# Kernel optimization log

Hardware: AMD Instinct MI355X
Metric: run time of the kernel (lower is better)

Reference implementation:

```python
import jax, jax.numpy as jnp
import numpy as np

B, T_OBS, T_FUT, D, H = 8192, 128, 64, 5, 128


def _gru_step(h, x, Wih, Whh, bih, bhh):
    # PyTorch GRU math, gate order (r, z, n) in the stacked [3H, *] weights.
    gi = x @ Wih.T + bih          # [B, 3H]
    gh = h @ Whh.T + bhh          # [B, 3H]
    ir, iz, inn = jnp.split(gi, 3, axis=-1)
    hr, hz, hn = jnp.split(gh, 3, axis=-1)
    r = jax.nn.sigmoid(ir + hr)
    z = jax.nn.sigmoid(iz + hz)
    n = jnp.tanh(inn + r * hn)
    return (1.0 - z) * n + z * h


def setup_inputs() -> dict:
    key = jax.random.key(0)
    ks = jax.random.split(key, 12)
    s = 0.1  # modest init scale to keep gates in a sane range
    return {
        "obs": jax.random.normal(ks[0], (B, T_OBS, D), jnp.float32),
        "target": jax.random.normal(ks[1], (B, T_FUT, D), jnp.float32),
        "enc_Wih": jax.random.normal(ks[2], (3 * H, D), jnp.float32) * s,
        "enc_Whh": jax.random.normal(ks[3], (3 * H, H), jnp.float32) * s,
        "enc_bih": jax.random.normal(ks[4], (3 * H,), jnp.float32) * s,
        "enc_bhh": jax.random.normal(ks[5], (3 * H,), jnp.float32) * s,
        "cell_Wih": jax.random.normal(ks[6], (3 * H, D), jnp.float32) * s,
        "cell_Whh": jax.random.normal(ks[7], (3 * H, H), jnp.float32) * s,
        "cell_bih": jax.random.normal(ks[8], (3 * H,), jnp.float32) * s,
        "cell_bhh": jax.random.normal(ks[9], (3 * H,), jnp.float32) * s,
        "head_W": jax.random.normal(ks[10], (D, H), jnp.float32) * s,
        "head_b": jax.random.normal(ks[11], (D,), jnp.float32) * s,
    }


def reference(obs, target, enc_Wih, enc_Whh, enc_bih, enc_bhh,
              cell_Wih, cell_Whh, cell_bih, cell_bhh, head_W, head_b):
    b = obs.shape[0]
    h0 = jnp.zeros((b, H), obs.dtype)

    # --- encoder: GRU over obs, keep only final hidden state ---
    def enc_step(h, x):
        h_new = _gru_step(h, x, enc_Wih, enc_Whh, enc_bih, enc_bhh)
        return h_new, None
    hT, _ = jax.lax.scan(enc_step, h0, jnp.swapaxes(obs, 0, 1))  # xs: [T_obs, B, D]

    # --- teacher-forced rollout: x_0 = obs[:, -1], x_t = target[:, t-1] ---
    xs = jnp.concatenate([obs[:, -1:, :], target[:, :-1, :]], axis=1)  # [B, T_fut, D]
    def roll_step(h, x):
        h_new = _gru_step(h, x, cell_Wih, cell_Whh, cell_bih, cell_bhh)
        return h_new, h_new
    _, hs = jax.lax.scan(roll_step, hT, jnp.swapaxes(xs, 0, 1))  # hs: [T_fut, B, H]

    preds = jnp.einsum('tbh,dh->tbd', hs, head_W) + head_b  # [T_fut, B, D]
    return jnp.swapaxes(preds, 0, 1)  # [B, T_fut, D]
```

## Files before the change

kernel.cpp:

```cpp
#include <hip/hip_runtime.h>

#define B_TOT 8192
#define T_OBS 128
#define T_FUT 64
#define T_ALL 192
#define DIN 5
#define HD 128
#define BT 32
#define LDSTR 136

#define LOG2E 1.44269504088896340736f

typedef __attribute__((ext_vector_type(8))) short short8;
typedef __attribute__((ext_vector_type(4))) float f32x4;
typedef __attribute__((ext_vector_type(2))) unsigned int u32x2;
typedef __attribute__((ext_vector_type(4))) unsigned int u32x4;

__device__ inline short f2bf(float f) {
    unsigned u = __float_as_uint(f);
    u += 0x7FFFu + ((u >> 16) & 1u);
    return (short)(u >> 16);
}

__device__ inline unsigned cvtpk(float lo, float hi) {
    unsigned r;
    asm volatile("v_cvt_pk_bf16_f32 %0, %1, %2" : "=v"(r) : "v"(lo), "v"(hi));
    return r;
}

__device__ inline f32x4 MFMA(short8 a, short8 b, f32x4 c) {
    return __builtin_amdgcn_mfma_f32_16x16x32_bf16(a, b, c, 0, 0, 0);
}

__device__ inline short8 load_w8s(const float* p, float s) {
    float4 a = *reinterpret_cast<const float4*>(p);
    float4 b = *reinterpret_cast<const float4*>(p + 4);
    short8 r;
    r[0] = f2bf(a.x * s); r[1] = f2bf(a.y * s); r[2] = f2bf(a.z * s); r[3] = f2bf(a.w * s);
    r[4] = f2bf(b.x * s); r[5] = f2bf(b.y * s); r[6] = f2bf(b.z * s); r[7] = f2bf(b.w * s);
    return r;
}
__device__ inline short8 load_w5s(const float* p, float s) {
    short8 r = (short8)0;
    r[0] = f2bf(p[0] * s); r[1] = f2bf(p[1] * s); r[2] = f2bf(p[2] * s);
    r[3] = f2bf(p[3] * s); r[4] = f2bf(p[4] * s);
    return r;
}

__global__ __launch_bounds__(512, 1)
void gru_tracemodel_kernel(const float* __restrict__ obs, const float* __restrict__ target,
                           const float* __restrict__ eWih, const float* __restrict__ eWhh,
                           const float* __restrict__ ebih, const float* __restrict__ ebhh,
                           const float* __restrict__ cWih, const float* __restrict__ cWhh,
                           const float* __restrict__ cbih, const float* __restrict__ cbhh,
                           const float* __restrict__ headW, const float* __restrict__ headb,
                           float* __restrict__ out)
{
    __shared__ __attribute__((aligned(16))) short Abuf[2][BT][LDSTR];

    const int tid   = threadIdx.x;
    const int wave  = tid >> 6;
    const int lane  = tid & 63;
    const int q     = lane >> 4;
    const int c     = lane & 15;
    const int b0    = blockIdx.x * BT;
    const int wbase = wave * 16;

    for (int i = tid; i < 2 * BT * LDSTR; i += 512) ((short*)Abuf)[i] = 0;

    short8 Wr[5], Wz[5], Wn[5];
    f32x4  br4, bz4, bnh4, bni4;

    auto load_phase = [&](const float* Wih, const float* Whh,
                          const float* bih, const float* bhh) {
        const int nr = 0 * HD + wbase + c;
        const int nz = 1 * HD + wbase + c;
        const int nn = 2 * HD + wbase + c;
        #pragma unroll
        for (int kt = 0; kt < 4; ++kt) {
            Wr[kt] = load_w8s(Whh + nr * HD + kt * 32 + q * 8, LOG2E);
            Wz[kt] = load_w8s(Whh + nz * HD + kt * 32 + q * 8, LOG2E);
            Wn[kt] = load_w8s(Whh + nn * HD + kt * 32 + q * 8, 2.f * LOG2E);
        }
        Wr[4] = (q == 0) ? load_w5s(Wih + nr * DIN, LOG2E) : (short8)0;
        Wz[4] = (q == 0) ? load_w5s(Wih + nz * DIN, LOG2E) : (short8)0;
        Wn[4] = (q == 0) ? load_w5s(Wih + nn * DIN, 2.f * LOG2E) : (short8)0;
        const int n0 = wbase + q * 4;
        #pragma unroll
        for (int r = 0; r < 4; ++r) {
            br4[r]  = (bih[0 * HD + n0 + r] + bhh[0 * HD + n0 + r]) * LOG2E;
            bz4[r]  = (bih[1 * HD + n0 + r] + bhh[1 * HD + n0 + r]) * LOG2E;
            bni4[r] = bih[2 * HD + n0 + r] * (2.f * LOG2E);
            bnh4[r] = bhh[2 * HD + n0 + r] * (2.f * LOG2E);
        }
    };
    load_phase(eWih, eWhh, ebih, ebhh);

    short8 Whd[4];
    f32x4  hb4;
    #pragma unroll
    for (int kt = 0; kt < 4; ++kt)
        Whd[kt] = (c < DIN) ? load_w8s(headW + c * HD + kt * 32 + q * 8, 1.f) : (short8)0;
    #pragma unroll
    for (int r = 0; r < 4; ++r)
        hb4[r] = (q * 4 + r < DIN) ? headb[q * 4 + r] : 0.f;

    float hreg[2][4] = {{0.f,0.f,0.f,0.f},{0.f,0.f,0.f,0.f}};

    const float* obsr[2] = { obs + (size_t)(b0 + c) * (T_OBS * DIN),
                             obs + (size_t)(b0 + 16 + c) * (T_OBS * DIN) };
    const float* tgtr[2] = { target + (size_t)(b0 + c) * (T_FUT * DIN),
                             target + (size_t)(b0 + 16 + c) * (T_FUT * DIN) };
    float x5[2][5] = {{0,0,0,0,0},{0,0,0,0,0}};
    if (q == 0) {
        #pragma unroll
        for (int a = 0; a < 2; ++a)
            #pragma unroll
            for (int j = 0; j < DIN; ++j) x5[a][j] = obsr[a][j];
    }

    for (int t = 0; t <= T_ALL; ++t) {
        __syncthreads();
        const int p = t & 1;

        short8 ah[2][4];
        #pragma unroll
        for (int a = 0; a < 2; ++a) {
            const short* ap = &Abuf[p][a * 16 + c][0];
            #pragma unroll
            for (int kt = 0; kt < 4; ++kt)
                ah[a][kt] = *reinterpret_cast<const short8*>(ap + kt * 32 + q * 8);
        }

        if (t >= T_OBS + 1 && wave == ((t - T_OBS - 1) & 7)) {
            const int s = t - (T_OBS + 1);
            const int d0 = q * 4;
            #pragma unroll
            for (int a = 0; a < 2; ++a) {
                f32x4 acc = hb4;
                #pragma unroll
                for (int kt = 0; kt < 4; ++kt)
                    acc = MFMA(Whd[kt], ah[a][kt], acc);
                if (d0 < DIN) {
                    float* op = out + ((size_t)(b0 + a * 16 + c) * T_FUT + s) * DIN + d0;
                    op[0] = acc[0];
                    if (q == 0) { op[1] = acc[1]; op[2] = acc[2]; op[3] = acc[3]; }
                }
            }
        }
        if (t == T_ALL) break;

        if (t == T_OBS) load_phase(cWih, cWhh, cbih, cbhh);

        short8 ax[2];
        {
            unsigned u0a = 0, u1a = 0, u2a = 0, u0b = 0, u1b = 0, u2b = 0;
            if (q == 0) {
                u0a = cvtpk(x5[0][0], x5[0][1]);
                u1a = cvtpk(x5[0][2], x5[0][3]);
                u2a = cvtpk(x5[0][4], 0.f);
                u0b = cvtpk(x5[1][0], x5[1][1]);
                u1b = cvtpk(x5[1][2], x5[1][3]);
                u2b = cvtpk(x5[1][4], 0.f);
            }
            u32x4 va = {u0a, u1a, u2a, 0u};
            u32x4 vb = {u0b, u1b, u2b, 0u};
            ax[0] = __builtin_bit_cast(short8, va);
            ax[1] = __builtin_bit_cast(short8, vb);
            const int tn = t + 1;
            if (q == 0 && tn < T_ALL) {
                #pragma unroll
                for (int a = 0; a < 2; ++a) {
                    const float* px = (tn < T_OBS)  ? (obsr[a] + tn * DIN)
                                    : (tn == T_OBS) ? (obsr[a] + (T_OBS - 1) * DIN)
                                                    : (tgtr[a] + (tn - T_OBS - 1) * DIN);
                    #pragma unroll
                    for (int j = 0; j < DIN; ++j) x5[a][j] = px[j];
                }
            }
        }

        #pragma unroll
        for (int a = 0; a < 2; ++a) {
            f32x4 aR  = br4;
            f32x4 aZ  = bz4;
            f32x4 aNh = bnh4;
            f32x4 aNi = bni4;
            #pragma unroll
            for (int kt = 0; kt < 4; ++kt) {
                aR  = MFMA(Wr[kt], ah[a][kt], aR);
                aZ  = MFMA(Wz[kt], ah[a][kt], aZ);
                aNh = MFMA(Wn[kt], ah[a][kt], aNh);
            }
            aR  = MFMA(Wr[4], ax[a], aR);
            aZ  = MFMA(Wz[4], ax[a], aZ);
            aNi = MFMA(Wn[4], ax[a], aNi);

            float hn[4];
            #pragma unroll
            for (int r = 0; r < 4; ++r) {
                float rv = __builtin_amdgcn_rcpf(1.f + __builtin_amdgcn_exp2f(-aR[r]));
                float zv = __builtin_amdgcn_rcpf(1.f + __builtin_amdgcn_exp2f(-aZ[r]));
                float yv = fmaf(rv, aNh[r], aNi[r]);
                float nv = 1.f - 2.f * __builtin_amdgcn_rcpf(1.f + __builtin_amdgcn_exp2f(yv));
                float h_ = nv + zv * (hreg[a][r] - nv);
                hreg[a][r] = h_;
                hn[r] = h_;
            }
            u32x2 wv = { cvtpk(hn[0], hn[1]), cvtpk(hn[2], hn[3]) };
            *reinterpret_cast<u32x2*>(&Abuf[1 - p][a * 16 + c][wbase + q * 4]) = wv;
        }
    }
}

extern "C" void kernel_launch(void* const* d_in, const int* in_sizes, int n_in,
                              void* d_out, int out_size, void* d_ws, size_t ws_size,
                              hipStream_t stream)
{
    (void)in_sizes; (void)n_in; (void)d_ws; (void)ws_size; (void)out_size;
    gru_tracemodel_kernel<<<dim3(B_TOT / BT), dim3(512), 0, stream>>>(
        (const float*)d_in[0],  (const float*)d_in[1],
        (const float*)d_in[2],  (const float*)d_in[3],
        (const float*)d_in[4],  (const float*)d_in[5],
        (const float*)d_in[6],  (const float*)d_in[7],
        (const float*)d_in[8],  (const float*)d_in[9],
        (const float*)d_in[10], (const float*)d_in[11],
        (float*)d_out);
}
```

Baseline: 338.1 us.

## Split waves by batch half and hidden slice; fuse GRU gate nonlinearities

```diff
diff --git a/kernel.cpp b/kernel.cpp
--- a/kernel.cpp
+++ b/kernel.cpp
@@ -64,34 +64,39 @@
     const int q     = lane >> 4;
     const int c     = lane & 15;
     const int b0    = blockIdx.x * BT;
-    const int wbase = wave * 16;
+    const int s4    = wave & 3;
+    const int a     = wave >> 2;
+    const int nbase = s4 * 32;
 
     for (int i = tid; i < 2 * BT * LDSTR; i += 512) ((short*)Abuf)[i] = 0;
 
-    short8 Wr[5], Wz[5], Wn[5];
-    f32x4  br4, bz4, bnh4, bni4;
+    short8 Wr[2][5], Wz[2][5], Wn[2][5];
+    f32x4  br4[2], bz4[2], bnh4[2], bni4[2];
 
     auto load_phase = [&](const float* Wih, const float* Whh,
                           const float* bih, const float* bhh) {
-        const int nr = 0 * HD + wbase + c;
-        const int nz = 1 * HD + wbase + c;
-        const int nn = 2 * HD + wbase + c;
-        #pragma unroll
-        for (int kt = 0; kt < 4; ++kt) {
-            Wr[kt] = load_w8s(Whh + nr * HD + kt * 32 + q * 8, LOG2E);
-            Wz[kt] = load_w8s(Whh + nz * HD + kt * 32 + q * 8, LOG2E);
-            Wn[kt] = load_w8s(Whh + nn * HD + kt * 32 + q * 8, 2.f * LOG2E);
-        }
-        Wr[4] = (q == 0) ? load_w5s(Wih + nr * DIN, LOG2E) : (short8)0;
-        Wz[4] = (q == 0) ? load_w5s(Wih + nz * DIN, LOG2E) : (short8)0;
-        Wn[4] = (q == 0) ? load_w5s(Wih + nn * DIN, 2.f * LOG2E) : (short8)0;
-        const int n0 = wbase + q * 4;
-        #pragma unroll
-        for (int r = 0; r < 4; ++r) {
-            br4[r]  = (bih[0 * HD + n0 + r] + bhh[0 * HD + n0 + r]) * LOG2E;
-            bz4[r]  = (bih[1 * HD + n0 + r] + bhh[1 * HD + n0 + r]) * LOG2E;
-            bni4[r] = bih[2 * HD + n0 + r] * (2.f * LOG2E);
-            bnh4[r] = bhh[2 * HD + n0 + r] * (2.f * LOG2E);
+        #pragma unroll
+        for (int g = 0; g < 2; ++g) {
+            const int nr = 0 * HD + nbase + 16 * g + c;
+            const int nz = 1 * HD + nbase + 16 * g + c;
+            const int nn = 2 * HD + nbase + 16 * g + c;
+            #pragma unroll
+            for (int kt = 0; kt < 4; ++kt) {
+                Wr[g][kt] = load_w8s(Whh + nr * HD + kt * 32 + q * 8, LOG2E);
+                Wz[g][kt] = load_w8s(Whh + nz * HD + kt * 32 + q * 8, LOG2E);
+                Wn[g][kt] = load_w8s(Whh + nn * HD + kt * 32 + q * 8, 2.f * LOG2E);
+            }
+            Wr[g][4] = (q == 0) ? load_w5s(Wih + nr * DIN, LOG2E) : (short8)0;
+            Wz[g][4] = (q == 0) ? load_w5s(Wih + nz * DIN, LOG2E) : (short8)0;
+            Wn[g][4] = (q == 0) ? load_w5s(Wih + nn * DIN, 2.f * LOG2E) : (short8)0;
+            const int n0 = nbase + 16 * g + q * 4;
+            #pragma unroll
+            for (int r = 0; r < 4; ++r) {
+                br4[g][r]  = (bih[0 * HD + n0 + r] + bhh[0 * HD + n0 + r]) * LOG2E;
+                bz4[g][r]  = (bih[1 * HD + n0 + r] + bhh[1 * HD + n0 + r]) * LOG2E;
+                bni4[g][r] = bih[2 * HD + n0 + r] * (2.f * LOG2E);
+                bnh4[g][r] = bhh[2 * HD + n0 + r] * (2.f * LOG2E);
+            }
         }
     };
     load_phase(eWih, eWhh, ebih, ebhh);
@@ -107,108 +112,95 @@
 
     float hreg[2][4] = {{0.f,0.f,0.f,0.f},{0.f,0.f,0.f,0.f}};
 
-    const float* obsr[2] = { obs + (size_t)(b0 + c) * (T_OBS * DIN),
-                             obs + (size_t)(b0 + 16 + c) * (T_OBS * DIN) };
-    const float* tgtr[2] = { target + (size_t)(b0 + c) * (T_FUT * DIN),
-                             target + (size_t)(b0 + 16 + c) * (T_FUT * DIN) };
-    float x5[2][5] = {{0,0,0,0,0},{0,0,0,0,0}};
+    const float* obsr = obs    + (size_t)(b0 + a * 16 + c) * (T_OBS * DIN);
+    const float* tgtr = target + (size_t)(b0 + a * 16 + c) * (T_FUT * DIN);
+    float x5[5] = {0, 0, 0, 0, 0};
     if (q == 0) {
         #pragma unroll
-        for (int a = 0; a < 2; ++a)
-            #pragma unroll
-            for (int j = 0; j < DIN; ++j) x5[a][j] = obsr[a][j];
+        for (int j = 0; j < DIN; ++j) x5[j] = obsr[j];
     }
 
     for (int t = 0; t <= T_ALL; ++t) {
         __syncthreads();
         const int p = t & 1;
 
-        short8 ah[2][4];
-        #pragma unroll
-        for (int a = 0; a < 2; ++a) {
-            const short* ap = &Abuf[p][a * 16 + c][0];
-            #pragma unroll
-            for (int kt = 0; kt < 4; ++kt)
-                ah[a][kt] = *reinterpret_cast<const short8*>(ap + kt * 32 + q * 8);
-        }
-
-        if (t >= T_OBS + 1 && wave == ((t - T_OBS - 1) & 7)) {
+        short8 ah[4];
+        const short* ap = &Abuf[p][a * 16 + c][0];
+        #pragma unroll
+        for (int kt = 0; kt < 4; ++kt)
+            ah[kt] = *reinterpret_cast<const short8*>(ap + kt * 32 + q * 8);
+
+        if (t >= T_OBS + 1 && s4 == ((t - T_OBS - 1) & 3)) {
             const int s = t - (T_OBS + 1);
             const int d0 = q * 4;
-            #pragma unroll
-            for (int a = 0; a < 2; ++a) {
-                f32x4 acc = hb4;
-                #pragma unroll
-                for (int kt = 0; kt < 4; ++kt)
-                    acc = MFMA(Whd[kt], ah[a][kt], acc);
-                if (d0 < DIN) {
-                    float* op = out + ((size_t)(b0 + a * 16 + c) * T_FUT + s) * DIN + d0;
-                    op[0] = acc[0];
-                    if (q == 0) { op[1] = acc[1]; op[2] = acc[2]; op[3] = acc[3]; }
-                }
+            f32x4 acc = hb4;
+            #pragma unroll
+            for (int kt = 0; kt < 4; ++kt)
+                acc = MFMA(Whd[kt], ah[kt], acc);
+            if (d0 < DIN) {
+                float* op = out + ((size_t)(b0 + a * 16 + c) * T_FUT + s) * DIN + d0;
+                op[0] = acc[0];
+                if (q == 0) { op[1] = acc[1]; op[2] = acc[2]; op[3] = acc[3]; }
             }
         }
         if (t == T_ALL) break;
 
         if (t == T_OBS) load_phase(cWih, cWhh, cbih, cbhh);
 
-        short8 ax[2];
+        short8 ax;
         {
-            unsigned u0a = 0, u1a = 0, u2a = 0, u0b = 0, u1b = 0, u2b = 0;
+            unsigned u0 = 0, u1 = 0, u2 = 0;
             if (q == 0) {
-                u0a = cvtpk(x5[0][0], x5[0][1]);
-                u1a = cvtpk(x5[0][2], x5[0][3]);
-                u2a = cvtpk(x5[0][4], 0.f);
-                u0b = cvtpk(x5[1][0], x5[1][1]);
-                u1b = cvtpk(x5[1][2], x5[1][3]);
-                u2b = cvtpk(x5[1][4], 0.f);
-            }
-            u32x4 va = {u0a, u1a, u2a, 0u};
-            u32x4 vb = {u0b, u1b, u2b, 0u};
-            ax[0] = __builtin_bit_cast(short8, va);
-            ax[1] = __builtin_bit_cast(short8, vb);
+                u0 = cvtpk(x5[0], x5[1]);
+                u1 = cvtpk(x5[2], x5[3]);
+                u2 = cvtpk(x5[4], 0.f);
+            }
+            u32x4 va = {u0, u1, u2, 0u};
+            ax = __builtin_bit_cast(short8, va);
             const int tn = t + 1;
             if (q == 0 && tn < T_ALL) {
+                const float* px = (tn < T_OBS)  ? (obsr + tn * DIN)
+                                : (tn == T_OBS) ? (obsr + (T_OBS - 1) * DIN)
+                                                : (tgtr + (tn - T_OBS - 1) * DIN);
                 #pragma unroll
-                for (int a = 0; a < 2; ++a) {
-                    const float* px = (tn < T_OBS)  ? (obsr[a] + tn * DIN)
-                                    : (tn == T_OBS) ? (obsr[a] + (T_OBS - 1) * DIN)
-                                                    : (tgtr[a] + (tn - T_OBS - 1) * DIN);
-                    #pragma unroll
-                    for (int j = 0; j < DIN; ++j) x5[a][j] = px[j];
-                }
-            }
-        }
-
-        #pragma unroll
-        for (int a = 0; a < 2; ++a) {
-            f32x4 aR  = br4;
-            f32x4 aZ  = bz4;
-            f32x4 aNh = bnh4;
-            f32x4 aNi = bni4;
-            #pragma unroll
-            for (int kt = 0; kt < 4; ++kt) {
-                aR  = MFMA(Wr[kt], ah[a][kt], aR);
-                aZ  = MFMA(Wz[kt], ah[a][kt], aZ);
-                aNh = MFMA(Wn[kt], ah[a][kt], aNh);
-            }
-            aR  = MFMA(Wr[4], ax[a], aR);
-            aZ  = MFMA(Wz[4], ax[a], aZ);
-            aNi = MFMA(Wn[4], ax[a], aNi);
+                for (int j = 0; j < DIN; ++j) x5[j] = px[j];
+            }
+        }
+
+        #pragma unroll
+        for (int g = 0; g < 2; ++g) {
+            f32x4 aR  = MFMA(Wr[g][0], ah[0], br4[g]);
+            f32x4 aZ  = MFMA(Wz[g][0], ah[0], bz4[g]);
+            f32x4 aNh = MFMA(Wn[g][0], ah[0], bnh4[g]);
+            #pragma unroll
+            for (int kt = 1; kt < 4; ++kt) {
+                aR  = MFMA(Wr[g][kt], ah[kt], aR);
+                aZ  = MFMA(Wz[g][kt], ah[kt], aZ);
+                aNh = MFMA(Wn[g][kt], ah[kt], aNh);
+            }
+            aR  = MFMA(Wr[g][4], ax, aR);
+            aZ  = MFMA(Wz[g][4], ax, aZ);
+            f32x4 aNi = MFMA(Wn[g][4], ax, bni4[g]);
 
             float hn[4];
             #pragma unroll
             for (int r = 0; r < 4; ++r) {
-                float rv = __builtin_amdgcn_rcpf(1.f + __builtin_amdgcn_exp2f(-aR[r]));
-                float zv = __builtin_amdgcn_rcpf(1.f + __builtin_amdgcn_exp2f(-aZ[r]));
-                float yv = fmaf(rv, aNh[r], aNi[r]);
-                float nv = 1.f - 2.f * __builtin_amdgcn_rcpf(1.f + __builtin_amdgcn_exp2f(yv));
-                float h_ = nv + zv * (hreg[a][r] - nv);
-                hreg[a][r] = h_;
+                float er  = __builtin_amdgcn_exp2f(-aR[r]);
+                float rv  = __builtin_amdgcn_rcpf(1.f + er);
+                float yv  = fmaf(rv, aNh[r], aNi[r]);
+                float ey  = __builtin_amdgcn_exp2f(yv);
+                float ez  = __builtin_amdgcn_exp2f(-aZ[r]);
+                float d2  = 1.f + ey;
+                float d1  = 1.f + ez;
+                float em1 = ey - 1.f;
+                float num = fmaf(ez, em1, hreg[g][r] * d2);
+                float h_  = num * __builtin_amdgcn_rcpf(d1 * d2);
+                hreg[g][r] = h_;
                 hn[r] = h_;
             }
             u32x2 wv = { cvtpk(hn[0], hn[1]), cvtpk(hn[2], hn[3]) };
-            *reinterpret_cast<u32x2*>(&Abuf[1 - p][a * 16 + c][wbase + q * 4]) = wv;
+            *reinterpret_cast<u32x2*>(
+                &Abuf[1 - p][a * 16 + c][nbase + 16 * g + q * 4]) = wv;
         }
     }
 }
```

After: 852.9 us. 2.52x slower.

## Split GRU time loop into phases and fuse gate reciprocals into one

Applied to the files above, without the earlier changes.

```diff
diff --git a/kernel.cpp b/kernel.cpp
--- a/kernel.cpp
+++ b/kernel.cpp
@@ -114,103 +114,128 @@
     float x5[2][5] = {{0,0,0,0,0},{0,0,0,0,0}};
     if (q == 0) {
         #pragma unroll
-        for (int a = 0; a < 2; ++a)
-            #pragma unroll
-            for (int j = 0; j < DIN; ++j) x5[a][j] = obsr[a][j];
+        for (int a = 0; a < 2; ++a) {
+            float4 v4 = *reinterpret_cast<const float4*>(obsr[a]);
+            x5[a][0] = v4.x; x5[a][1] = v4.y; x5[a][2] = v4.z; x5[a][3] = v4.w;
+            x5[a][4] = obsr[a][4];
+        }
     }
 
-    for (int t = 0; t <= T_ALL; ++t) {
-        __syncthreads();
-        const int p = t & 1;
-
-        short8 ah[2][4];
+#define GRU_STEP(T, DO_HEAD, ENC)                                              \
+  {                                                                            \
+    __syncthreads();                                                           \
+    const int p_ = (T) & 1;                                                    \
+    short8 ah[2][4];                                                           \
+    _Pragma("unroll")                                                          \
+    for (int a = 0; a < 2; ++a) {                                              \
+      const short* ap = &Abuf[p_][a * 16 + c][0];                              \
+      _Pragma("unroll")                                                        \
+      for (int kt = 0; kt < 4; ++kt)                                           \
+        ah[a][kt] = *reinterpret_cast<const short8*>(ap + kt * 32 + q * 8);    \
+    }                                                                          \
+    if (DO_HEAD) {                                                             \
+      const int s_ = (T) - (T_OBS + 1);                                        \
+      if (wave == (s_ & 7)) {                                                  \
+        const int d0 = q * 4;                                                  \
+        _Pragma("unroll")                                                      \
+        for (int a = 0; a < 2; ++a) {                                          \
+          f32x4 acc = hb4;                                                     \
+          _Pragma("unroll")                                                    \
+          for (int kt = 0; kt < 4; ++kt)                                       \
+            acc = MFMA(Whd[kt], ah[a][kt], acc);                               \
+          if (d0 < DIN) {                                                      \
+            float* op = out + ((size_t)(b0 + a * 16 + c) * T_FUT + s_) * DIN + d0; \
+            op[0] = acc[0];                                                    \
+            if (q == 0) { op[1] = acc[1]; op[2] = acc[2]; op[3] = acc[3]; }    \
+          }                                                                    \
+        }                                                                      \
+      }                                                                        \
+    }                                                                          \
+    short8 ax[2];                                                              \
+    {                                                                          \
+      u32x4 va = { cvtpk(x5[0][0], x5[0][1]), cvtpk(x5[0][2], x5[0][3]),       \
+                   cvtpk(x5[0][4], 0.f), 0u };                                 \
+      u32x4 vb = { cvtpk(x5[1][0], x5[1][1]), cvtpk(x5[1][2], x5[1][3]),       \
+                   cvtpk(x5[1][4], 0.f), 0u };                                 \
+      ax[0] = __builtin_bit_cast(short8, va);                                  \
+      ax[1] = __builtin_bit_cast(short8, vb);                                  \
+      if (q == 0) {                                                            \
+        const int tn_ = (T) + 1;                                               \
+        _Pragma("unroll")                                                      \
+        for (int a = 0; a < 2; ++a) {                                          \
+          const float* px = (ENC)                                              \
+              ? (obsr[a] + ((tn_ < T_OBS) ? tn_ : (T_OBS - 1)) * DIN)          \
+              : (tgtr[a] + (tn_ - T_OBS - 1) * DIN);                           \
+          float4 v4 = *reinterpret_cast<const float4*>(px);                    \
+          x5[a][0] = v4.x; x5[a][1] = v4.y; x5[a][2] = v4.z; x5[a][3] = v4.w;  \
+          x5[a][4] = px[4];                                                    \
+        }                                                                      \
+      }                                                                        \
+    }                                                                          \
+    _Pragma("unroll")                                                          \
+    for (int a = 0; a < 2; ++a) {                                              \
+      f32x4 aR  = MFMA(Wr[0], ah[a][0], br4);                                  \
+      f32x4 aZ  = MFMA(Wz[0], ah[a][0], bz4);                                  \
+      f32x4 aNh = MFMA(Wn[0], ah[a][0], bnh4);                                 \
+      _Pragma("unroll")                                                        \
+      for (int kt = 1; kt < 4; ++kt) {                                         \
+        aR  = MFMA(Wr[kt], ah[a][kt], aR);                                     \
+        aZ  = MFMA(Wz[kt], ah[a][kt], aZ);                                     \
+        aNh = MFMA(Wn[kt], ah[a][kt], aNh);                                    \
+      }                                                                        \
+      aR  = MFMA(Wr[4], ax[a], aR);                                            \
+      aZ  = MFMA(Wz[4], ax[a], aZ);                                            \
+      f32x4 aNi = MFMA(Wn[4], ax[a], bni4);                                    \
+      float hn[4];                                                             \
+      _Pragma("unroll")                                                        \
+      for (int r = 0; r < 4; ++r) {                                            \
+        float er  = __builtin_amdgcn_exp2f(-aR[r]);                            \
+        float rv  = __builtin_amdgcn_rcpf(1.f + er);                           \
+        float yv  = fmaf(rv, aNh[r], aNi[r]);                                  \
+        float ey  = __builtin_amdgcn_exp2f(yv);                                \
+        float ez  = __builtin_amdgcn_exp2f(-aZ[r]);                            \
+        float d2  = 1.f + ey;                                                  \
+        float d1  = 1.f + ez;                                                  \
+        float em1 = ey - 1.f;                                                  \
+        float num = fmaf(ez, em1, hreg[a][r] * d2);                            \
+        float h_  = num * __builtin_amdgcn_rcpf(d1 * d2);                      \
+        hreg[a][r] = h_;                                                       \
+        hn[r] = h_;                                                            \
+      }                                                                        \
+      u32x2 wv = { cvtpk(hn[0], hn[1]), cvtpk(hn[2], hn[3]) };                 \
+      *reinterpret_cast<u32x2*>(&Abuf[1 - p_][a * 16 + c][wbase + q * 4]) = wv;\
+    }                                                                          \
+  }
+
+    for (int t = 0; t < T_OBS; ++t) GRU_STEP(t, 0, 1);
+
+    load_phase(cWih, cWhh, cbih, cbhh);
+    GRU_STEP(T_OBS, 0, 0);
+
+    for (int t = T_OBS + 1; t < T_ALL; ++t) GRU_STEP(t, 1, 0);
+
+    __syncthreads();
+    if (wave == ((T_FUT - 1) & 7)) {
+        const int p_ = T_ALL & 1;
+        const int s_ = T_FUT - 1;
+        const int d0 = q * 4;
         #pragma unroll
         for (int a = 0; a < 2; ++a) {
-            const short* ap = &Abuf[p][a * 16 + c][0];
-            #pragma unroll
-            for (int kt = 0; kt < 4; ++kt)
-                ah[a][kt] = *reinterpret_cast<const short8*>(ap + kt * 32 + q * 8);
-        }
-
-        if (t >= T_OBS + 1 && wave == ((t - T_OBS - 1) & 7)) {
-            const int s = t - (T_OBS + 1);
-            const int d0 = q * 4;
-            #pragma unroll
-            for (int a = 0; a < 2; ++a) {
-                f32x4 acc = hb4;
-                #pragma unroll
-                for (int kt = 0; kt < 4; ++kt)
-                    acc = MFMA(Whd[kt], ah[a][kt], acc);
-                if (d0 < DIN) {
-                    float* op = out + ((size_t)(b0 + a * 16 + c) * T_FUT + s) * DIN + d0;
-                    op[0] = acc[0];
-                    if (q == 0) { op[1] = acc[1]; op[2] = acc[2]; op[3] = acc[3]; }
-                }
-            }
-        }
-        if (t == T_ALL) break;
-
-        if (t == T_OBS) load_phase(cWih, cWhh, cbih, cbhh);
-
-        short8 ax[2];
-        {
-            unsigned u0a = 0, u1a = 0, u2a = 0, u0b = 0, u1b = 0, u2b = 0;
-            if (q == 0) {
-                u0a = cvtpk(x5[0][0], x5[0][1]);
-                u1a = cvtpk(x5[0][2], x5[0][3]);
-                u2a = cvtpk(x5[0][4], 0.f);
-                u0b = cvtpk(x5[1][0], x5[1][1]);
-                u1b = cvtpk(x5[1][2], x5[1][3]);
-                u2b = cvtpk(x5[1][4], 0.f);
-            }
-            u32x4 va = {u0a, u1a, u2a, 0u};
-            u32x4 vb = {u0b, u1b, u2b, 0u};
-            ax[0] = __builtin_bit_cast(short8, va);
-            ax[1] = __builtin_bit_cast(short8, vb);
-            const int tn = t + 1;
-            if (q == 0 && tn < T_ALL) {
-                #pragma unroll
-                for (int a = 0; a < 2; ++a) {
-                    const float* px = (tn < T_OBS)  ? (obsr[a] + tn * DIN)
-                                    : (tn == T_OBS) ? (obsr[a] + (T_OBS - 1) * DIN)
-                                                    : (tgtr[a] + (tn - T_OBS - 1) * DIN);
-                    #pragma unroll
-                    for (int j = 0; j < DIN; ++j) x5[a][j] = px[j];
-                }
-            }
-        }
-
-        #pragma unroll
-        for (int a = 0; a < 2; ++a) {
-            f32x4 aR  = br4;
-            f32x4 aZ  = bz4;
-            f32x4 aNh = bnh4;
-            f32x4 aNi = bni4;
+            const short* ap = &Abuf[p_][a * 16 + c][0];
+            f32x4 acc = hb4;
             #pragma unroll
             for (int kt = 0; kt < 4; ++kt) {
-                aR  = MFMA(Wr[kt], ah[a][kt], aR);
-                aZ  = MFMA(Wz[kt], ah[a][kt], aZ);
-                aNh = MFMA(Wn[kt], ah[a][kt], aNh);
+                short8 h8 = *reinterpret_cast<const short8*>(ap + kt * 32 + q * 8);
+                acc = MFMA(Whd[kt], h8, acc);
             }
-            aR  = MFMA(Wr[4], ax[a], aR);
-            aZ  = MFMA(Wz[4], ax[a], aZ);
-            aNi = MFMA(Wn[4], ax[a], aNi);
-
-            float hn[4];
-            #pragma unroll
-            for (int r = 0; r < 4; ++r) {
-                float rv = __builtin_amdgcn_rcpf(1.f + __builtin_amdgcn_exp2f(-aR[r]));
-                float zv = __builtin_amdgcn_rcpf(1.f + __builtin_amdgcn_exp2f(-aZ[r]));
-                float yv = fmaf(rv, aNh[r], aNi[r]);
-                float nv = 1.f - 2.f * __builtin_amdgcn_rcpf(1.f + __builtin_amdgcn_exp2f(yv));
-                float h_ = nv + zv * (hreg[a][r] - nv);
-                hreg[a][r] = h_;
-                hn[r] = h_;
+            if (d0 < DIN) {
+                float* op = out + ((size_t)(b0 + a * 16 + c) * T_FUT + s_) * DIN + d0;
+                op[0] = acc[0];
+                if (q == 0) { op[1] = acc[1]; op[2] = acc[2]; op[3] = acc[3]; }
             }
-            u32x2 wv = { cvtpk(hn[0], hn[1]), cvtpk(hn[2], hn[3]) };
-            *reinterpret_cast<u32x2*>(&Abuf[1 - p][a * 16 + c][wbase + q * 4]) = wv;
         }
     }
+#undef GRU_STEP
 }
 
 extern "C" void kernel_launch(void* const* d_in, const int* in_sizes, int n_in,
```

After: 322.5 us (median of 2 runs). 1.05x faster.
